# Kernel optimization log

Measured on AMD Instinct MI355X. Metric: run time of the kernel, lower is better.

The kernel has to match this reference:

```python
import jax, jax.numpy as jnp
import numpy as np

B, S, T = 64, 512, 256  # batch, seq_len, num_tags


def setup_inputs() -> dict:
    key = jax.random.key(0)
    k1, k2, k3, k4 = jax.random.split(key, 4)
    emissions = jax.random.normal(k1, (B, S, T), dtype=jnp.float32)
    tags = jax.random.randint(k2, (B, S), 0, T, dtype=jnp.int32)
    mask = jnp.ones((B, S), dtype=bool)
    # nn.init.uniform_(-0.01, 0.01) as in reset_parameters()
    transitions = jax.random.uniform(k3, (T, T), minval=-0.01, maxval=0.01, dtype=jnp.float32)
    tse = jax.random.uniform(k4, (T + 2, T + 2), minval=-0.01, maxval=0.01, dtype=jnp.float32)
    tse = tse.at[T + 1, T].set(-10000.0)  # transitions[end_tag, start_tag] = -10000
    return {"emissions": emissions, "tags": tags, "mask": mask,
            "transitions": transitions, "transitions_with_start_end": tse}


def reference(emissions, tags, mask, transitions, transitions_with_start_end):
    Bv, Sv, Tv = emissions.shape
    start, end = Tv, Tv + 1

    # ---- forward algorithm (log partition), faithful to the torch recurrence:
    # new[b, j] = alpha[b, j] + logsumexp_k( trans[k, j] + emit_t[b, k] )
    # (the mask line fv*mask + fv*~mask in the original is a no-op)
    alpha0 = emissions[:, 0] + transitions_with_start_end[start, :Tv]

    def step(alpha, em_t):  # em_t: [B, T]
        lse = jax.nn.logsumexp(transitions[None, :, :] + em_t[:, :, None], axis=1)  # [B, T]
        return alpha + lse, None

    ems = jnp.swapaxes(emissions[:, 1:], 0, 1)  # [S-1, B, T]
    alpha, _ = jax.lax.scan(step, alpha0, ems)
    forward_score = jax.nn.logsumexp(alpha + transitions_with_start_end[:Tv, end], axis=1)  # [B]

    # ---- gold path score
    mf = mask.astype(emissions.dtype)
    emit = jnp.take_along_axis(emissions, tags[:, :, None].astype(jnp.int32), axis=2)[:, :, 0]  # [B, S]
    score = transitions_with_start_end[start, tags[:, 0]]
    score = score + jnp.sum(emit * mf, axis=1)
    score = score + jnp.sum(transitions[tags[:, 1:], tags[:, :-1]] * mf[:, 1:], axis=1)
    last_idx = jnp.sum(mask.astype(jnp.int32), axis=1) - 1  # [B]
    last_tags = jnp.take_along_axis(tags, last_idx[:, None], axis=1)[:, 0]
    score = score + transitions_with_start_end[last_tags, end]

    return forward_score - score  # negative log-likelihood per batch element, [B]
```

## Files before the change

### kernel.cpp

```cpp
#include <hip/hip_runtime.h>
#include <cstdint>

#define B_ 64
#define S_ 512
#define T_ 256
#define TP2 258

#define BM 64
#define BK 32
#define LDA 40
#define LDB 40

typedef __attribute__((ext_vector_type(8))) short short8;
typedef __attribute__((ext_vector_type(4))) float f32x4;

__device__ __forceinline__ ushort f2bf(float f) {
    union { float f; uint32_t u; } c; c.f = f;
    uint32_t u = c.u;
    u += 0x7FFFu + ((u >> 16) & 1u);
    return (ushort)(u >> 16);
}

__global__ void prep_w(const float* __restrict__ trans, ushort* __restrict__ wt,
                       float* __restrict__ accb) {
    int k = blockIdx.x;
    int n = threadIdx.x;
    wt[n * T_ + k] = f2bf(__expf(trans[k * T_ + n]));
    if (k < B_) accb[k * T_ + n] = 0.f;
}

__global__ __launch_bounds__(256, 3) void gemm_lse(
    const float* __restrict__ em, const ushort* __restrict__ wt,
    float* __restrict__ accb)
{
    __shared__ ushort Alds[BM * LDA];
    __shared__ ushort Blds[T_ * LDB];

    int blk  = blockIdx.x;
    long r0  = (long)blk * BM;
    int batch = blk >> 3;
    bool has_s0 = (blk & 7) == 0;

    int tid  = threadIdx.x;
    int wave = tid >> 6;
    int lane = tid & 63;
    int quad = lane >> 4;
    int l15  = lane & 15;

    f32x4 acc[4][4];
    #pragma unroll
    for (int i = 0; i < 4; ++i)
        #pragma unroll
        for (int j = 0; j < 4; ++j)
            acc[i][j] = (f32x4){0.f, 0.f, 0.f, 0.f};

    int srow = tid >> 2;
    int skc  = (tid & 3) * 8;

    for (int kt = 0; kt < T_ / BK; ++kt) {
        int k0 = kt * BK;
        {
            const float* src = em + (r0 + srow) * T_ + k0 + skc;
            float4 va = *(const float4*)(src);
            float4 vb = *(const float4*)(src + 4);
            union { ushort u[8]; uint4 v; } pk;
            pk.u[0] = f2bf(__expf(va.x)); pk.u[1] = f2bf(__expf(va.y));
            pk.u[2] = f2bf(__expf(va.z)); pk.u[3] = f2bf(__expf(va.w));
            pk.u[4] = f2bf(__expf(vb.x)); pk.u[5] = f2bf(__expf(vb.y));
            pk.u[6] = f2bf(__expf(vb.z)); pk.u[7] = f2bf(__expf(vb.w));
            *(uint4*)&Alds[srow * LDA + skc] = pk.v;
        }
        #pragma unroll
        for (int p = 0; p < 4; ++p) {
            int idx = tid + p * 256;
            uint4 v = *(const uint4*)&wt[(idx >> 2) * T_ + k0 + (idx & 3) * 8];
            *(uint4*)&Blds[(idx >> 2) * LDB + (idx & 3) * 8] = v;
        }
        __syncthreads();

        short8 af[4], bf[4];
        #pragma unroll
        for (int i = 0; i < 4; ++i)
            af[i] = *(const short8*)&Alds[(i * 16 + l15) * LDA + quad * 8];
        #pragma unroll
        for (int j = 0; j < 4; ++j)
            bf[j] = *(const short8*)&Blds[(wave * 64 + j * 16 + l15) * LDB + quad * 8];
        #pragma unroll
        for (int i = 0; i < 4; ++i)
            #pragma unroll
            for (int j = 0; j < 4; ++j)
                acc[i][j] = __builtin_amdgcn_mfma_f32_16x16x32_bf16(af[i], bf[j], acc[i][j], 0, 0, 0);
        __syncthreads();
    }

    #pragma unroll
    for (int j = 0; j < 4; ++j) {
        float s = 0.f;
        #pragma unroll
        for (int i = 0; i < 4; ++i) {
            f32x4 a = acc[i][j];
            #pragma unroll
            for (int v = 0; v < 4; ++v) {
                bool skip = has_s0 && (i == 0) && (quad == 0) && (v == 0);
                if (!skip) s += __logf(a[v]);
            }
        }
        s += __shfl_xor(s, 16);
        s += __shfl_xor(s, 32);
        if (lane < 16)
            atomicAdd(&accb[batch * T_ + wave * 64 + j * 16 + lane], s);
    }
}

__global__ __launch_bounds__(256) void finalize(
    const float* __restrict__ em, const int* __restrict__ tags,
    const float* __restrict__ trans, const float* __restrict__ tse,
    const float* __restrict__ accb, float* __restrict__ out)
{
    __shared__ float red[8];
    int b = blockIdx.x;
    int j = threadIdx.x;
    int w = j >> 6;

    float v = em[(long)b * S_ * T_ + j] + tse[T_ * TP2 + j]
            + accb[b * T_ + j] + tse[j * TP2 + (T_ + 1)];

    float m = v;
    #pragma unroll
    for (int o = 32; o; o >>= 1) m = fmaxf(m, __shfl_xor(m, o));
    if ((j & 63) == 0) red[w] = m;
    __syncthreads();
    m = fmaxf(fmaxf(red[0], red[1]), fmaxf(red[2], red[3]));

    float e = __expf(v - m);
    #pragma unroll
    for (int o = 32; o; o >>= 1) e += __shfl_xor(e, o);
    if ((j & 63) == 0) red[4 + w] = e;
    __syncthreads();
    float fwd = m + __logf(red[4] + red[5] + red[6] + red[7]);

    const int* tg = tags + b * S_;
    float sc = 0.f;
    for (int s = j; s < S_; s += 256) {
        int t = tg[s];
        sc += em[((long)b * S_ + s) * T_ + t];
        if (s >= 1) sc += trans[t * T_ + tg[s - 1]];
    }
    if (j == 0) {
        sc += tse[T_ * TP2 + tg[0]];
        sc += tse[tg[S_ - 1] * TP2 + (T_ + 1)];
    }
    #pragma unroll
    for (int o = 32; o; o >>= 1) sc += __shfl_xor(sc, o);
    __syncthreads();
    if ((j & 63) == 0) red[w] = sc;
    __syncthreads();
    if (j == 0) out[b] = fwd - (red[0] + red[1] + red[2] + red[3]);
}

extern "C" void kernel_launch(void* const* d_in, const int* in_sizes, int n_in,
                              void* d_out, int out_size, void* d_ws, size_t ws_size,
                              hipStream_t stream) {
    const float* em    = (const float*)d_in[0];
    const int*   tags  = (const int*)d_in[1];
    const float* trans = (const float*)d_in[3];
    const float* tse   = (const float*)d_in[4];
    float* out = (float*)d_out;

    ushort* wt   = (ushort*)d_ws;
    float*  accb = (float*)((char*)d_ws + 131072);

    prep_w<<<T_, T_, 0, stream>>>(trans, wt, accb);
    gemm_lse<<<(B_ * S_) / BM, 256, 0, stream>>>(em, wt, accb);
    finalize<<<B_, T_, 0, stream>>>(em, tags, trans, tse, accb, out);
}
```

Baseline: 93.04 us.

## Stage whole A tile in LDS once and read B fragments directly from global

The row tile shrinks from 64 to 32 rows and the whole exp/bf16-converted emission tile is staged into LDS in a single pass, stored in MFMA fragment order. This replaces the per-k-step double __syncthreads loop. The B operand (exp of transitions) is no longer staged through LDS; each wave loads its fragments straight from global memory, relying on L2/L1 caching. This removes most barriers and LDS traffic and doubles the grid for occupancy, but B reuse per block halves and global loads now sit on the MFMA critical path.

After: 101.0 us. +8.5%, slower.

```diff
diff --git a/kernel.cpp b/kernel.cpp
--- a/kernel.cpp
+++ b/kernel.cpp
@@ -6,10 +6,7 @@
 #define T_ 256
 #define TP2 258
 
-#define BM 64
-#define BK 32
-#define LDA 40
-#define LDB 40
+#define BM 32
 
 typedef __attribute__((ext_vector_type(8))) short short8;
 typedef __attribute__((ext_vector_type(4))) float f32x4;
@@ -29,75 +26,65 @@
     if (k < B_) accb[k * T_ + n] = 0.f;
 }
 
-__global__ __launch_bounds__(256, 3) void gemm_lse(
+__global__ __launch_bounds__(256, 4) void gemm_lse(
     const float* __restrict__ em, const ushort* __restrict__ wt,
     float* __restrict__ accb)
 {
-    __shared__ ushort Alds[BM * LDA];
-    __shared__ ushort Blds[T_ * LDB];
+    __shared__ alignas(16) ushort Afrag[8 * 2 * 512];
 
-    int blk  = blockIdx.x;
-    long r0  = (long)blk * BM;
-    int batch = blk >> 3;
-    bool has_s0 = (blk & 7) == 0;
+    int blk   = blockIdx.x;
+    long r0   = (long)blk * BM;
+    int batch = blk >> 4;
+    bool has_s0 = (blk & 15) == 0;
 
     int tid  = threadIdx.x;
-    int wave = tid >> 6;
+    int wv   = tid >> 6;
     int lane = tid & 63;
     int quad = lane >> 4;
     int l15  = lane & 15;
+    int n0   = wv * 64;
 
-    f32x4 acc[4][4];
     #pragma unroll
-    for (int i = 0; i < 4; ++i)
+    for (int q = 0; q < 4; ++q) {
+        int s   = tid + q * 256;
+        int row = s >> 5;
+        int kq  = s & 31;
+        const float* src = em + (r0 + row) * T_ + kq * 8;
+        float4 va = *(const float4*)(src);
+        float4 vb = *(const float4*)(src + 4);
+        union { ushort u[8]; uint4 v; } pk;
+        pk.u[0] = f2bf(__expf(va.x)); pk.u[1] = f2bf(__expf(va.y));
+        pk.u[2] = f2bf(__expf(va.z)); pk.u[3] = f2bf(__expf(va.w));
+        pk.u[4] = f2bf(__expf(vb.x)); pk.u[5] = f2bf(__expf(vb.y));
+        pk.u[6] = f2bf(__expf(vb.z)); pk.u[7] = f2bf(__expf(vb.w));
+        int kt = kq >> 2, qd = kq & 3, ih = row >> 4, rl = row & 15;
+        *(uint4*)&Afrag[kt * 1024 + ih * 512 + (qd * 16 + rl) * 8] = pk.v;
+    }
+    __syncthreads();
+
+    f32x4 acc[2][4];
+    #pragma unroll
+    for (int i = 0; i < 2; ++i)
         #pragma unroll
         for (int j = 0; j < 4; ++j)
             acc[i][j] = (f32x4){0.f, 0.f, 0.f, 0.f};
 
-    int srow = tid >> 2;
-    int skc  = (tid & 3) * 8;
-
-    for (int kt = 0; kt < T_ / BK; ++kt) {
-        int k0 = kt * BK;
-        {
-            const float* src = em + (r0 + srow) * T_ + k0 + skc;
-            float4 va = *(const float4*)(src);
-            float4 vb = *(const float4*)(src + 4);
-            union { ushort u[8]; uint4 v; } pk;
-            pk.u[0] = f2bf(__expf(va.x)); pk.u[1] = f2bf(__expf(va.y));
-            pk.u[2] = f2bf(__expf(va.z)); pk.u[3] = f2bf(__expf(va.w));
-            pk.u[4] = f2bf(__expf(vb.x)); pk.u[5] = f2bf(__expf(vb.y));
-            pk.u[6] = f2bf(__expf(vb.z)); pk.u[7] = f2bf(__expf(vb.w));
-            *(uint4*)&Alds[srow * LDA + skc] = pk.v;
+    for (int kt = 0; kt < 8; ++kt) {
+        short8 af0 = *(const short8*)&Afrag[kt * 1024 + lane * 8];
+        short8 af1 = *(const short8*)&Afrag[kt * 1024 + 512 + lane * 8];
+        #pragma unroll
+        for (int j = 0; j < 4; ++j) {
+            short8 bf = *(const short8*)&wt[(n0 + j * 16 + l15) * T_ + kt * 32 + quad * 8];
+            acc[0][j] = __builtin_amdgcn_mfma_f32_16x16x32_bf16(af0, bf, acc[0][j], 0, 0, 0);
+            acc[1][j] = __builtin_amdgcn_mfma_f32_16x16x32_bf16(af1, bf, acc[1][j], 0, 0, 0);
         }
-        #pragma unroll
-        for (int p = 0; p < 4; ++p) {
-            int idx = tid + p * 256;
-            uint4 v = *(const uint4*)&wt[(idx >> 2) * T_ + k0 + (idx & 3) * 8];
-            *(uint4*)&Blds[(idx >> 2) * LDB + (idx & 3) * 8] = v;
-        }
-        __syncthreads();
-
-        short8 af[4], bf[4];
-        #pragma unroll
-        for (int i = 0; i < 4; ++i)
-            af[i] = *(const short8*)&Alds[(i * 16 + l15) * LDA + quad * 8];
-        #pragma unroll
-        for (int j = 0; j < 4; ++j)
-            bf[j] = *(const short8*)&Blds[(wave * 64 + j * 16 + l15) * LDB + quad * 8];
-        #pragma unroll
-        for (int i = 0; i < 4; ++i)
-            #pragma unroll
-            for (int j = 0; j < 4; ++j)
-                acc[i][j] = __builtin_amdgcn_mfma_f32_16x16x32_bf16(af[i], bf[j], acc[i][j], 0, 0, 0);
-        __syncthreads();
     }
 
     #pragma unroll
     for (int j = 0; j < 4; ++j) {
         float s = 0.f;
         #pragma unroll
-        for (int i = 0; i < 4; ++i) {
+        for (int i = 0; i < 2; ++i) {
             f32x4 a = acc[i][j];
             #pragma unroll
             for (int v = 0; v < 4; ++v) {
@@ -108,7 +95,7 @@
         s += __shfl_xor(s, 16);
         s += __shfl_xor(s, 32);
         if (lane < 16)
-            atomicAdd(&accb[batch * T_ + wave * 64 + j * 16 + lane], s);
+            atomicAdd(&accb[batch * T_ + n0 + j * 16 + lane], s);
     }
 }
 
```

## Fuse transition exp into GEMM, preload A fragments, replace atomics with partials

Applied to the files above, without the earlier changes.

Drops the separate prep_w kernel. Each wave now reads fp32 transitions directly from global memory and applies exp and bf16 conversion in registers for its B fragments, and the whole 64x256 exp(emission) tile is staged once into LDS in MFMA fragment order. This removes the per-k-tile barriers. Per-block partial sums are written to a workspace instead of being atomically added, and finalize sums the 8 partials per batch, so the zeroing step is no longer needed. The trade-off is redundant exp work on the transition matrix in every block and strided, uncoalesced-per-lane global loads for B. Occupancy is also lowered to 2 blocks.

Result: slower. 97.32 us (+4.6%).

```diff
diff --git a/kernel.cpp b/kernel.cpp
--- a/kernel.cpp
+++ b/kernel.cpp
@@ -7,9 +7,6 @@
 #define TP2 258
 
 #define BM 64
-#define BK 32
-#define LDA 40
-#define LDB 40
 
 typedef __attribute__((ext_vector_type(8))) short short8;
 typedef __attribute__((ext_vector_type(4))) float f32x4;
@@ -21,31 +18,44 @@
     return (ushort)(u >> 16);
 }
 
-__global__ void prep_w(const float* __restrict__ trans, ushort* __restrict__ wt,
-                       float* __restrict__ accb) {
-    int k = blockIdx.x;
-    int n = threadIdx.x;
-    wt[n * T_ + k] = f2bf(__expf(trans[k * T_ + n]));
-    if (k < B_) accb[k * T_ + n] = 0.f;
-}
-
-__global__ __launch_bounds__(256, 3) void gemm_lse(
-    const float* __restrict__ em, const ushort* __restrict__ wt,
-    float* __restrict__ accb)
+__global__ __launch_bounds__(256, 2) void gemm_lse(
+    const float* __restrict__ em, const float* __restrict__ trans,
+    float* __restrict__ accP)
 {
-    __shared__ ushort Alds[BM * LDA];
-    __shared__ ushort Blds[T_ * LDB];
+    __shared__ alignas(16) ushort Afrag[8 * 4 * 64 * 8];
 
     int blk  = blockIdx.x;
     long r0  = (long)blk * BM;
-    int batch = blk >> 3;
     bool has_s0 = (blk & 7) == 0;
 
     int tid  = threadIdx.x;
-    int wave = tid >> 6;
+    int wv   = tid >> 6;
     int lane = tid & 63;
-    int quad = lane >> 4;
+    int qd   = lane >> 4;
     int l15  = lane & 15;
+    int n0   = wv * 64;
+
+    {
+        int kq   = tid & 31;
+        int skt  = kq >> 2;
+        int squd = kq & 3;
+        int rb   = tid >> 5;
+        #pragma unroll
+        for (int q = 0; q < 8; ++q) {
+            int row = rb + q * 8;
+            const float* src = em + (r0 + row) * T_ + kq * 8;
+            float4 va = *(const float4*)(src);
+            float4 vb = *(const float4*)(src + 4);
+            union { ushort u[8]; uint4 v; } pk;
+            pk.u[0] = f2bf(__expf(va.x)); pk.u[1] = f2bf(__expf(va.y));
+            pk.u[2] = f2bf(__expf(va.z)); pk.u[3] = f2bf(__expf(va.w));
+            pk.u[4] = f2bf(__expf(vb.x)); pk.u[5] = f2bf(__expf(vb.y));
+            pk.u[6] = f2bf(__expf(vb.z)); pk.u[7] = f2bf(__expf(vb.w));
+            int i = row >> 4, rl = row & 15;
+            *(uint4*)&Afrag[(skt * 256 + i * 64 + squd * 16 + rl) * 8] = pk.v;
+        }
+    }
+    __syncthreads();
 
     f32x4 acc[4][4];
     #pragma unroll
@@ -54,43 +64,30 @@
         for (int j = 0; j < 4; ++j)
             acc[i][j] = (f32x4){0.f, 0.f, 0.f, 0.f};
 
-    int srow = tid >> 2;
-    int skc  = (tid & 3) * 8;
+    for (int kt = 0; kt < 8; ++kt) {
+        short8 af[4];
+        #pragma unroll
+        for (int i = 0; i < 4; ++i)
+            af[i] = *(const short8*)&Afrag[(kt * 256 + i * 64 + lane) * 8];
 
-    for (int kt = 0; kt < T_ / BK; ++kt) {
-        int k0 = kt * BK;
-        {
-            const float* src = em + (r0 + srow) * T_ + k0 + skc;
-            float4 va = *(const float4*)(src);
-            float4 vb = *(const float4*)(src + 4);
-            union { ushort u[8]; uint4 v; } pk;
-            pk.u[0] = f2bf(__expf(va.x)); pk.u[1] = f2bf(__expf(va.y));
-            pk.u[2] = f2bf(__expf(va.z)); pk.u[3] = f2bf(__expf(va.w));
-            pk.u[4] = f2bf(__expf(vb.x)); pk.u[5] = f2bf(__expf(vb.y));
-            pk.u[6] = f2bf(__expf(vb.z)); pk.u[7] = f2bf(__expf(vb.w));
-            *(uint4*)&Alds[srow * LDA + skc] = pk.v;
+        float bx[4][8];
+        #pragma unroll
+        for (int j = 0; j < 4; ++j) {
+            const float* bp = trans + (kt * 32 + qd * 8) * T_ + n0 + j * 16 + l15;
+            #pragma unroll
+            for (int ii = 0; ii < 8; ++ii)
+                bx[j][ii] = bp[ii * T_];
         }
         #pragma unroll
-        for (int p = 0; p < 4; ++p) {
-            int idx = tid + p * 256;
-            uint4 v = *(const uint4*)&wt[(idx >> 2) * T_ + k0 + (idx & 3) * 8];
-            *(uint4*)&Blds[(idx >> 2) * LDB + (idx & 3) * 8] = v;
+        for (int j = 0; j < 4; ++j) {
+            union { ushort u[8]; short8 v; } bw;
+            #pragma unroll
+            for (int ii = 0; ii < 8; ++ii)
+                bw.u[ii] = f2bf(__expf(bx[j][ii]));
+            #pragma unroll
+            for (int i = 0; i < 4; ++i)
+                acc[i][j] = __builtin_amdgcn_mfma_f32_16x16x32_bf16(af[i], bw.v, acc[i][j], 0, 0, 0);
         }
-        __syncthreads();
-
-        short8 af[4], bf[4];
-        #pragma unroll
-        for (int i = 0; i < 4; ++i)
-            af[i] = *(const short8*)&Alds[(i * 16 + l15) * LDA + quad * 8];
-        #pragma unroll
-        for (int j = 0; j < 4; ++j)
-            bf[j] = *(const short8*)&Blds[(wave * 64 + j * 16 + l15) * LDB + quad * 8];
-        #pragma unroll
-        for (int i = 0; i < 4; ++i)
-            #pragma unroll
-            for (int j = 0; j < 4; ++j)
-                acc[i][j] = __builtin_amdgcn_mfma_f32_16x16x32_bf16(af[i], bf[j], acc[i][j], 0, 0, 0);
-        __syncthreads();
     }
 
     #pragma unroll
@@ -101,29 +98,34 @@
             f32x4 a = acc[i][j];
             #pragma unroll
             for (int v = 0; v < 4; ++v) {
-                bool skip = has_s0 && (i == 0) && (quad == 0) && (v == 0);
+                bool skip = has_s0 && (i == 0) && (qd == 0) && (v == 0);
                 if (!skip) s += __logf(a[v]);
             }
         }
         s += __shfl_xor(s, 16);
         s += __shfl_xor(s, 32);
         if (lane < 16)
-            atomicAdd(&accb[batch * T_ + wave * 64 + j * 16 + lane], s);
+            accP[blk * T_ + n0 + j * 16 + lane] = s;
     }
 }
 
 __global__ __launch_bounds__(256) void finalize(
     const float* __restrict__ em, const int* __restrict__ tags,
     const float* __restrict__ trans, const float* __restrict__ tse,
-    const float* __restrict__ accb, float* __restrict__ out)
+    const float* __restrict__ accP, float* __restrict__ out)
 {
     __shared__ float red[8];
     int b = blockIdx.x;
     int j = threadIdx.x;
     int w = j >> 6;
 
+    float p = 0.f;
+    #pragma unroll
+    for (int q = 0; q < 8; ++q)
+        p += accP[((b << 3) + q) * T_ + j];
+
     float v = em[(long)b * S_ * T_ + j] + tse[T_ * TP2 + j]
-            + accb[b * T_ + j] + tse[j * TP2 + (T_ + 1)];
+            + p + tse[j * TP2 + (T_ + 1)];
 
     float m = v;
     #pragma unroll
@@ -167,10 +169,8 @@
     const float* tse   = (const float*)d_in[4];
     float* out = (float*)d_out;
 
-    ushort* wt   = (ushort*)d_ws;
-    float*  accb = (float*)((char*)d_ws + 131072);
+    float* accP = (float*)d_ws;
 
-    prep_w<<<T_, T_, 0, stream>>>(trans, wt, accb);
-    gemm_lse<<<(B_ * S_) / BM, 256, 0, stream>>>(em, wt, accb);
-    finalize<<<B_, T_, 0, stream>>>(em, tags, trans, tse, accb, out);
+    gemm_lse<<<(B_ * S_) / BM, 256, 0, stream>>>(em, trans, accP);
+    finalize<<<B_, T_, 0, stream>>>(em, tags, trans, tse, accP, out);
 }
```
